# Optimization experiments

Hardware: AMD Instinct MI355X
Metric: run time of the kernel (lower is better)

The kernel has to match this reference:

```python
import jax, jax.numpy as jnp
import numpy as np

B, IN, OUT = 64, 4096, 1024
BETA, THRESH, RESET = 0.98, 0.4, 0.0
A_POS, A_NEG, TRACE_DECAY = 0.005, 0.004, 0.85


def setup_inputs() -> dict:
    key = jax.random.key(0)
    k1, k2 = jax.random.split(key)
    in_spikes = jax.random.uniform(k1, (B, IN), dtype=jnp.float32)  # spike input currents
    weight = jax.random.normal(k2, (OUT, IN), dtype=jnp.float32) * 0.02  # nn.Linear weight [out,in]
    membrane = jnp.zeros((B, OUT), dtype=jnp.float32)
    trace_pre = jnp.zeros((IN,), dtype=jnp.float32)
    trace_post = jnp.zeros((OUT,), dtype=jnp.float32)
    return {"in_spikes": in_spikes, "weight": weight, "membrane": membrane,
            "trace_pre": trace_pre, "trace_post": trace_post}


def reference(in_spikes, weight, membrane, trace_pre, trace_post):
    # weighted input: [B,OUT]
    weighted = in_spikes @ weight.T
    # LIF neuron update
    mem = membrane * BETA + weighted
    spikes = (mem > THRESH).astype(mem.dtype)
    mem = jnp.where(spikes > 0, RESET, mem)
    # STDP trace updates (trace_pre broadcasts [IN] -> [B,IN], as in the torch code)
    tp = jnp.clip(trace_pre * TRACE_DECAY + in_spikes, 0.0, 1.0)   # [B,IN]
    tq = jnp.clip(trace_post * TRACE_DECAY + spikes, 0.0, 1.0)     # [B,OUT]
    # potentiation - depression = (a_pos - a_neg) * outer(tp, tq); summed over batch
    # and transposed -> [OUT,IN]. Expressed as one einsum instead of materializing
    # the [B,IN,OUT] tensor (algebraically identical).
    dw = (A_POS - A_NEG) * jnp.einsum('bi,bo->oi', tp, tq)
    w_new = jnp.clip(weight + dw, -0.1, 0.5)
    # module returns out_spikes; state updates returned too for verification
    return spikes, mem, w_new, tp, tq
```

## Files before the change

### kernel.cpp

```cpp
#include <hip/hip_runtime.h>


#define B_    64
#define IN_   4096
#define OUT_  1024
#define SPLITS 32
#define KC    128
#define BK    64

static constexpr int OFF_SPIKES = 0;
static constexpr int OFF_MEM    = B_ * OUT_;
static constexpr int OFF_W      = 2 * B_ * OUT_;
static constexpr int OFF_TP     = OFF_W + OUT_ * IN_;
static constexpr int OFF_TQ     = OFF_TP + B_ * IN_;

__global__ __launch_bounds__(256) void k_gemm1(const float* __restrict__ A,
                                               const float* __restrict__ Wt,
                                               float* __restrict__ part) {
  const int nb = blockIdx.x;
  const int ks = blockIdx.y;
  const int t  = threadIdx.x;

  __shared__ float At[BK][64];
  __shared__ float Wn[BK][64];

  const int col4 = t & 15;
  const int rowg = t >> 4;
  const int bu   = t >> 4;
  const int nv   = t & 15;

  float acc[4][4];
#pragma unroll
  for (int u = 0; u < 4; ++u)
#pragma unroll
    for (int v = 0; v < 4; ++v) acc[u][v] = 0.f;

#pragma unroll
  for (int c = 0; c < KC / BK; ++c) {
    const int k0 = ks * KC + c * BK;

    float4 av[4], wv[4];
#pragma unroll
    for (int p = 0; p < 4; ++p) {
      const int r = rowg + p * 16;
      av[p] = *reinterpret_cast<const float4*>(A  + (size_t)r * IN_ + k0 + col4 * 4);
      wv[p] = *reinterpret_cast<const float4*>(Wt + (size_t)(nb * 64 + r) * IN_ + k0 + col4 * 4);
    }

    if (c) __syncthreads();

    const int sw = 2 * col4;
#pragma unroll
    for (int p = 0; p < 4; ++p) {
      const int r = rowg + p * 16;
      const int cA = r ^ sw;
      At[col4 * 4 + 0][cA] = av[p].x;
      At[col4 * 4 + 1][cA] = av[p].y;
      At[col4 * 4 + 2][cA] = av[p].z;
      At[col4 * 4 + 3][cA] = av[p].w;
      Wn[col4 * 4 + 0][cA] = wv[p].x;
      Wn[col4 * 4 + 1][cA] = wv[p].y;
      Wn[col4 * 4 + 2][cA] = wv[p].z;
      Wn[col4 * 4 + 3][cA] = wv[p].w;
    }
    __syncthreads();

#pragma unroll
    for (int kq = 0; kq < BK / 4; ++kq) {
      const int sH = (2 * kq) & 28;
      const int tt = (2 * kq) & 2;
#pragma unroll
      for (int m = 0; m < 4; ++m) {
        const int kk = kq * 4 + m;
        const float4 a4 = *reinterpret_cast<const float4*>(&At[kk][(bu * 4) ^ sH]);
        const float4 w4 = *reinterpret_cast<const float4*>(&Wn[kk][(nv * 4) ^ sH]);
        const float aa[4] = {a4.x, a4.y, a4.z, a4.w};
        const float ww[4] = {w4.x, w4.y, w4.z, w4.w};
#pragma unroll
        for (int u = 0; u < 4; ++u)
#pragma unroll
          for (int v = 0; v < 4; ++v)
            acc[u][v] = fmaf(aa[u ^ (tt ? 2 : 0)], ww[v ^ (tt ? 2 : 0)], acc[u][v]);
      }
    }
  }

#pragma unroll
  for (int u = 0; u < 4; ++u) {
    const int b = bu * 4 + u;
    float4 r;
    r.x = acc[u][0]; r.y = acc[u][1]; r.z = acc[u][2]; r.w = acc[u][3];
    *reinterpret_cast<float4*>(
        part + ((size_t)(ks * 64 + b)) * OUT_ + nb * 64 + nv * 4) = r;
  }
}

__global__ __launch_bounds__(256) void k_lif(const float* __restrict__ part,
                                             const float* __restrict__ membrane,
                                             const float* __restrict__ trace_post,
                                             float* __restrict__ out) {
  const int t = blockIdx.x * 256 + threadIdx.x;
  const int b = t >> 10;
  const int n = t & (OUT_ - 1);

  float s0 = 0.f, s1 = 0.f, s2 = 0.f, s3 = 0.f;
#pragma unroll
  for (int ks = 0; ks < SPLITS; ks += 4) {
    s0 += part[((size_t)((ks + 0) * B_ + b)) * OUT_ + n];
    s1 += part[((size_t)((ks + 1) * B_ + b)) * OUT_ + n];
    s2 += part[((size_t)((ks + 2) * B_ + b)) * OUT_ + n];
    s3 += part[((size_t)((ks + 3) * B_ + b)) * OUT_ + n];
  }
  const float weighted = (s0 + s1) + (s2 + s3);

  const float mem   = fmaf(membrane[t], 0.98f, weighted);
  const float spike = (mem > 0.4f) ? 1.0f : 0.0f;
  const float memo  = (spike > 0.0f) ? 0.0f : mem;
  float tq = fmaf(trace_post[n], 0.85f, spike);
  tq = fminf(fmaxf(tq, 0.0f), 1.0f);

  out[OFF_SPIKES + t] = spike;
  out[OFF_MEM    + t] = memo;
  out[OFF_TQ     + t] = tq;
}

__global__ __launch_bounds__(256) void k_tp(const float* __restrict__ in_spikes,
                                            const float* __restrict__ trace_pre,
                                            float* __restrict__ out) {
  const int t  = blockIdx.x * 256 + threadIdx.x;
  const int i4 = t & (IN_ / 4 - 1);
  const float4 x  = reinterpret_cast<const float4*>(in_spikes)[t];
  const float4 tr = reinterpret_cast<const float4*>(trace_pre)[i4];
  float4 r;
  r.x = fminf(fmaxf(fmaf(tr.x, 0.85f, x.x), 0.0f), 1.0f);
  r.y = fminf(fmaxf(fmaf(tr.y, 0.85f, x.y), 0.0f), 1.0f);
  r.z = fminf(fmaxf(fmaf(tr.z, 0.85f, x.z), 0.0f), 1.0f);
  r.w = fminf(fmaxf(fmaf(tr.w, 0.85f, x.w), 0.0f), 1.0f);
  reinterpret_cast<float4*>(out + OFF_TP)[t] = r;
}

__global__ __launch_bounds__(256) void k_wnew(const float* __restrict__ weight,
                                              const float* __restrict__ tp,
                                              const float* __restrict__ tq,
                                              float* __restrict__ wout) {
  const int i0 = blockIdx.x * 64;
  const int o0 = blockIdx.y * 64;

  __shared__ float tpl[64][68];
  __shared__ float tql[64][68];
  {
    const int c4 = threadIdx.x & 15;
    const int rr = threadIdx.x >> 4;
#pragma unroll
    for (int r = 0; r < 4; ++r) {
      const int b = rr + r * 16;
      *reinterpret_cast<float4*>(&tpl[b][c4 * 4]) =
          *reinterpret_cast<const float4*>(tp + (size_t)b * IN_  + i0 + c4 * 4);
      *reinterpret_cast<float4*>(&tql[b][c4 * 4]) =
          *reinterpret_cast<const float4*>(tq + (size_t)b * OUT_ + o0 + c4 * 4);
    }
  }
  __syncthreads();

  const int il = threadIdx.x & 15;
  const int ol = threadIdx.x >> 4;

  float acc[4][4];
#pragma unroll
  for (int u = 0; u < 4; ++u)
#pragma unroll
    for (int v = 0; v < 4; ++v) acc[u][v] = 0.f;

#pragma unroll 4
  for (int b = 0; b < 64; ++b) {
    const float4 tpv = *reinterpret_cast<const float4*>(&tpl[b][il * 4]);
    const float4 tqv = *reinterpret_cast<const float4*>(&tql[b][ol * 4]);
    const float tp4[4] = {tpv.x, tpv.y, tpv.z, tpv.w};
    const float tq4[4] = {tqv.x, tqv.y, tqv.z, tqv.w};
#pragma unroll
    for (int u = 0; u < 4; ++u)
#pragma unroll
      for (int v = 0; v < 4; ++v)
        acc[u][v] = fmaf(tq4[u], tp4[v], acc[u][v]);
  }

  const float cdw = (float)(0.005 - 0.004);
#pragma unroll
  for (int u = 0; u < 4; ++u) {
    const int o = o0 + ol * 4 + u;
    const float4 wv = *reinterpret_cast<const float4*>(
        weight + (size_t)o * IN_ + i0 + il * 4);
    float4 r;
    r.x = fminf(fmaxf(fmaf(cdw, acc[u][0], wv.x), -0.1f), 0.5f);
    r.y = fminf(fmaxf(fmaf(cdw, acc[u][1], wv.y), -0.1f), 0.5f);
    r.z = fminf(fmaxf(fmaf(cdw, acc[u][2], wv.z), -0.1f), 0.5f);
    r.w = fminf(fmaxf(fmaf(cdw, acc[u][3], wv.w), -0.1f), 0.5f);
    *reinterpret_cast<float4*>(wout + (size_t)o * IN_ + i0 + il * 4) = r;
  }
}

extern "C" void kernel_launch(void* const* d_in, const int* in_sizes, int n_in,
                              void* d_out, int out_size, void* d_ws, size_t ws_size,
                              hipStream_t stream) {
  const float* in_spikes  = (const float*)d_in[0];
  const float* weight     = (const float*)d_in[1];
  const float* membrane   = (const float*)d_in[2];
  const float* trace_pre  = (const float*)d_in[3];
  const float* trace_post = (const float*)d_in[4];
  float* out = (float*)d_out;

  float* part = out + OFF_W;

  k_gemm1<<<dim3(16, SPLITS), 256, 0, stream>>>(in_spikes, weight, part);
  k_tp   <<<dim3(256),        256, 0, stream>>>(in_spikes, trace_pre, out);
  k_lif  <<<dim3(256),        256, 0, stream>>>(part, membrane, trace_post, out);
  k_wnew <<<dim3(64, 16),     256, 0, stream>>>(weight, out + OFF_TP,
                                                out + OFF_TQ, out + OFF_W);
}
```

Measured before the change: 98.50 us.

## Rework split-K GEMM to 64 splits with 8x4 register tiles and fuse trace kernels

The first GEMM now uses 64 K-splits of one 64-wide chunk each, run by 128-thread blocks. Each thread computes an 8x4 output tile instead of a 4x4 one, and the inner chunk loop and its extra barrier are gone. The trace_pre update kernel is merged into the LIF reduction kernel, which saves one launch. The cost is that the reduction now reads twice as many partial sums from global memory, and each block has fewer threads.

```diff
diff --git a/kernel.cpp b/kernel.cpp
--- a/kernel.cpp
+++ b/kernel.cpp
@@ -4,17 +4,16 @@
 #define B_    64
 #define IN_   4096
 #define OUT_  1024
-#define SPLITS 32
-#define KC    128
+#define SPLITS 64
 #define BK    64
 
 static constexpr int OFF_SPIKES = 0;
 static constexpr int OFF_MEM    = B_ * OUT_;
 static constexpr int OFF_W      = 2 * B_ * OUT_;
 static constexpr int OFF_TP     = OFF_W + OUT_ * IN_;
-static constexpr int OFF_TQ     = OFF_TP + B_ * IN_;
-
-__global__ __launch_bounds__(256) void k_gemm1(const float* __restrict__ A,
+static constexpr int OFF_TQ    = OFF_TP + B_ * IN_;
+
+__global__ __launch_bounds__(128) void k_gemm1(const float* __restrict__ A,
                                                const float* __restrict__ Wt,
                                                float* __restrict__ part) {
   const int nb = blockIdx.x;
@@ -26,79 +25,80 @@
 
   const int col4 = t & 15;
   const int rowg = t >> 4;
-  const int bu   = t >> 4;
-  const int nv   = t & 15;
-
-  float acc[4][4];
-#pragma unroll
-  for (int u = 0; u < 4; ++u)
+  const int k0   = ks * BK;
+
+  float4 av[8], wv[8];
+#pragma unroll
+  for (int p = 0; p < 8; ++p) {
+    const int r = rowg + p * 8;
+    av[p] = *reinterpret_cast<const float4*>(A  + (size_t)r * IN_ + k0 + col4 * 4);
+    wv[p] = *reinterpret_cast<const float4*>(Wt + (size_t)(nb * 64 + r) * IN_ + k0 + col4 * 4);
+  }
+
+  const int sw = 2 * col4;
+#pragma unroll
+  for (int p = 0; p < 8; ++p) {
+    const int r  = rowg + p * 8;
+    const int cA = r ^ sw;
+    At[col4 * 4 + 0][cA] = av[p].x;
+    At[col4 * 4 + 1][cA] = av[p].y;
+    At[col4 * 4 + 2][cA] = av[p].z;
+    At[col4 * 4 + 3][cA] = av[p].w;
+    Wn[col4 * 4 + 0][cA] = wv[p].x;
+    Wn[col4 * 4 + 1][cA] = wv[p].y;
+    Wn[col4 * 4 + 2][cA] = wv[p].z;
+    Wn[col4 * 4 + 3][cA] = wv[p].w;
+  }
+  __syncthreads();
+
+  const int bu8 = t >> 4;
+  const int nv4 = t & 15;
+
+  float acc[8][4];
+#pragma unroll
+  for (int u = 0; u < 8; ++u)
 #pragma unroll
     for (int v = 0; v < 4; ++v) acc[u][v] = 0.f;
 
 #pragma unroll
-  for (int c = 0; c < KC / BK; ++c) {
-    const int k0 = ks * KC + c * BK;
-
-    float4 av[4], wv[4];
-#pragma unroll
-    for (int p = 0; p < 4; ++p) {
-      const int r = rowg + p * 16;
-      av[p] = *reinterpret_cast<const float4*>(A  + (size_t)r * IN_ + k0 + col4 * 4);
-      wv[p] = *reinterpret_cast<const float4*>(Wt + (size_t)(nb * 64 + r) * IN_ + k0 + col4 * 4);
-    }
-
-    if (c) __syncthreads();
-
-    const int sw = 2 * col4;
-#pragma unroll
-    for (int p = 0; p < 4; ++p) {
-      const int r = rowg + p * 16;
-      const int cA = r ^ sw;
-      At[col4 * 4 + 0][cA] = av[p].x;
-      At[col4 * 4 + 1][cA] = av[p].y;
-      At[col4 * 4 + 2][cA] = av[p].z;
-      At[col4 * 4 + 3][cA] = av[p].w;
-      Wn[col4 * 4 + 0][cA] = wv[p].x;
-      Wn[col4 * 4 + 1][cA] = wv[p].y;
-      Wn[col4 * 4 + 2][cA] = wv[p].z;
-      Wn[col4 * 4 + 3][cA] = wv[p].w;
-    }
-    __syncthreads();
-
-#pragma unroll
-    for (int kq = 0; kq < BK / 4; ++kq) {
-      const int sH = (2 * kq) & 28;
-      const int tt = (2 * kq) & 2;
-#pragma unroll
-      for (int m = 0; m < 4; ++m) {
-        const int kk = kq * 4 + m;
-        const float4 a4 = *reinterpret_cast<const float4*>(&At[kk][(bu * 4) ^ sH]);
-        const float4 w4 = *reinterpret_cast<const float4*>(&Wn[kk][(nv * 4) ^ sH]);
-        const float aa[4] = {a4.x, a4.y, a4.z, a4.w};
-        const float ww[4] = {w4.x, w4.y, w4.z, w4.w};
-#pragma unroll
-        for (int u = 0; u < 4; ++u)
-#pragma unroll
-          for (int v = 0; v < 4; ++v)
-            acc[u][v] = fmaf(aa[u ^ (tt ? 2 : 0)], ww[v ^ (tt ? 2 : 0)], acc[u][v]);
+  for (int kq = 0; kq < BK / 4; ++kq) {
+    const int sH = (2 * kq) & 28;
+    const int xe = (kq & 1) ? 2 : 0;
+#pragma unroll
+    for (int m = 0; m < 4; ++m) {
+      const int kk = kq * 4 + m;
+      const float4 a0 = *reinterpret_cast<const float4*>(&At[kk][(bu8 * 8 + 0) ^ sH]);
+      const float4 a1 = *reinterpret_cast<const float4*>(&At[kk][(bu8 * 8 + 4) ^ sH]);
+      const float4 w4 = *reinterpret_cast<const float4*>(&Wn[kk][(nv4 * 4) ^ sH]);
+      const float a0e[4] = {a0.x, a0.y, a0.z, a0.w};
+      const float a1e[4] = {a1.x, a1.y, a1.z, a1.w};
+      const float we [4] = {w4.x, w4.y, w4.z, w4.w};
+#pragma unroll
+      for (int u = 0; u < 8; ++u) {
+        const float au = (u < 4) ? a0e[(u ^ xe) & 3] : a1e[((u - 4) ^ xe) & 3];
+#pragma unroll
+        for (int v = 0; v < 4; ++v)
+          acc[u][v] = fmaf(au, we[(v ^ xe) & 3], acc[u][v]);
       }
     }
   }
 
 #pragma unroll
-  for (int u = 0; u < 4; ++u) {
-    const int b = bu * 4 + u;
+  for (int u = 0; u < 8; ++u) {
+    const int b = bu8 * 8 + u;
     float4 r;
     r.x = acc[u][0]; r.y = acc[u][1]; r.z = acc[u][2]; r.w = acc[u][3];
     *reinterpret_cast<float4*>(
-        part + ((size_t)(ks * 64 + b)) * OUT_ + nb * 64 + nv * 4) = r;
-  }
-}
-
-__global__ __launch_bounds__(256) void k_lif(const float* __restrict__ part,
-                                             const float* __restrict__ membrane,
-                                             const float* __restrict__ trace_post,
-                                             float* __restrict__ out) {
+        part + ((size_t)(ks * 64 + b)) * OUT_ + nb * 64 + nv4 * 4) = r;
+  }
+}
+
+__global__ __launch_bounds__(256) void k_post(const float* __restrict__ part,
+                                              const float* __restrict__ membrane,
+                                              const float* __restrict__ trace_post,
+                                              const float* __restrict__ in_spikes,
+                                              const float* __restrict__ trace_pre,
+                                              float* __restrict__ out) {
   const int t = blockIdx.x * 256 + threadIdx.x;
   const int b = t >> 10;
   const int n = t & (OUT_ - 1);
@@ -122,12 +122,7 @@
   out[OFF_SPIKES + t] = spike;
   out[OFF_MEM    + t] = memo;
   out[OFF_TQ     + t] = tq;
-}
-
-__global__ __launch_bounds__(256) void k_tp(const float* __restrict__ in_spikes,
-                                            const float* __restrict__ trace_pre,
-                                            float* __restrict__ out) {
-  const int t  = blockIdx.x * 256 + threadIdx.x;
+
   const int i4 = t & (IN_ / 4 - 1);
   const float4 x  = reinterpret_cast<const float4*>(in_spikes)[t];
   const float4 tr = reinterpret_cast<const float4*>(trace_pre)[i4];
@@ -211,9 +206,9 @@
 
   float* part = out + OFF_W;
 
-  k_gemm1<<<dim3(16, SPLITS), 256, 0, stream>>>(in_spikes, weight, part);
-  k_tp   <<<dim3(256),        256, 0, stream>>>(in_spikes, trace_pre, out);
-  k_lif  <<<dim3(256),        256, 0, stream>>>(part, membrane, trace_post, out);
+  k_gemm1<<<dim3(16, SPLITS), 128, 0, stream>>>(in_spikes, weight, part);
+  k_post <<<dim3(256),        256, 0, stream>>>(part, membrane, trace_post,
+                                                in_spikes, trace_pre, out);
   k_wnew <<<dim3(64, 16),     256, 0, stream>>>(weight, out + OFF_TP,
                                                 out + OFF_TQ, out + OFF_W);
 }
```

Measured after the change: 101.4 us. 1.03x slower.
